# Kernel tuning notes

Hardware: AMD Instinct MI355X
Metric: run time of the kernel (lower is better)

The kernel has to match this reference:

```python
import jax, jax.numpy as jnp
import numpy as np

N_NODES = 100_000
N_EDGES = 1_600_000
N_GRAPHS = 512
D_NODE = 128
H = 128
L_EXTRA = 2  # model_layer - 1


def _bn(x, g, b, eps=1e-5):
    # BatchNorm1d, training-mode math (biased batch variance), eval dropout = identity
    mu = jnp.mean(x, axis=0)
    var = jnp.var(x, axis=0)
    return g * (x - mu) * jax.lax.rsqrt(var + eps) + b


def _gin_conv(x, src, dst, W1, b1, bng, bnb, W2, b2):
    # GINConv (eps=0): mlp(x + sum_{j->i} x_j); mlp = Lin -> BN -> ReLU -> Lin
    agg = jax.ops.segment_sum(x[src], dst, num_segments=x.shape[0])
    h = x + agg
    h = jax.nn.relu(_bn(h @ W1 + b1, bng, bnb))
    return h @ W2 + b2


def setup_inputs():
    key = jax.random.key(0)
    ks = jax.random.split(key, 24)
    s = 0.05
    d = {}
    d["x"] = jax.random.normal(ks[0], (N_NODES, D_NODE), dtype=jnp.float32)
    d["edge_index"] = jax.random.randint(ks[1], (2, N_EDGES), 0, N_NODES, dtype=jnp.int32)
    d["batch"] = jnp.sort(jax.random.randint(ks[2], (N_NODES,), 0, N_GRAPHS, dtype=jnp.int32))
    d["vn_emb"] = jax.random.normal(ks[3], (1, H)) * s
    # conv1 MLP: Linear(D_NODE, 2H) -> BN -> ReLU -> Linear(2H, H)
    d["c1_W1"] = jax.random.normal(ks[4], (D_NODE, 2 * H)) * s
    d["c1_b1"] = jnp.zeros((2 * H,))
    d["c1_bng"] = jnp.ones((2 * H,))
    d["c1_bnb"] = jnp.zeros((2 * H,))
    d["c1_W2"] = jax.random.normal(ks[5], (2 * H, H)) * s
    d["c1_b2"] = jnp.zeros((H,))
    d["bn1_g"] = jnp.ones((H,))
    d["bn1_b"] = jnp.zeros((H,))
    # stacked extra GIN layers (model_layer - 1)
    d["cW1"] = jax.random.normal(ks[6], (L_EXTRA, H, 2 * H)) * s
    d["cb1"] = jnp.zeros((L_EXTRA, 2 * H))
    d["cbng"] = jnp.ones((L_EXTRA, 2 * H))
    d["cbnb"] = jnp.zeros((L_EXTRA, 2 * H))
    d["cW2"] = jax.random.normal(ks[7], (L_EXTRA, 2 * H, H)) * s
    d["cb2"] = jnp.zeros((L_EXTRA, H))
    d["bns_g"] = jnp.ones((L_EXTRA, H))
    d["bns_b"] = jnp.zeros((L_EXTRA, H))
    # virtual node MLP: Lin(H,2H)->BN->ReLU->Lin(2H,H)->BN->ReLU->Dropout
    d["vW1"] = jax.random.normal(ks[8], (H, 2 * H)) * s
    d["vb1"] = jnp.zeros((2 * H,))
    d["vbn1_g"] = jnp.ones((2 * H,))
    d["vbn1_b"] = jnp.zeros((2 * H,))
    d["vW2"] = jax.random.normal(ks[9], (2 * H, H)) * s
    d["vb2"] = jnp.zeros((H,))
    d["vbn2_g"] = jnp.ones((H,))
    d["vbn2_b"] = jnp.zeros((H,))
    return d


def reference(x, edge_index, batch, vn_emb, c1_W1, c1_b1, c1_bng, c1_bnb, c1_W2, c1_b2,
              bn1_g, bn1_b, cW1, cb1, cbng, cbnb, cW2, cb2, bns_g, bns_b,
              vW1, vb1, vbn1_g, vbn1_b, vW2, vb2, vbn2_g, vbn2_b):
    src, dst = edge_index[0], edge_index[1]
    # virtual node feature per graph: Embedding(1, H) indexed with zeros
    vfeat = jnp.broadcast_to(vn_emb[0], (N_GRAPHS, H))
    # layer 1: dropout is identity in eval mode
    post = jax.nn.relu(_bn(_gin_conv(x, src, dst, c1_W1, c1_b1, c1_bng, c1_bnb, c1_W2, c1_b2), bn1_g, bn1_b))
    for i in range(L_EXTRA):
        post = post + vfeat[batch]                       # virtual-node broadcast
        post = _bn(_gin_conv(post, src, dst, cW1[i], cb1[i], cbng[i], cbnb[i], cW2[i], cb2[i]), bns_g[i], bns_b[i])
        if i < L_EXTRA - 1:
            post = jax.nn.relu(post)
            pooled = jax.ops.segment_sum(post, batch, num_segments=N_GRAPHS)  # GlobalAddPool
            z = pooled + vfeat
            z = jax.nn.relu(_bn(z @ vW1 + vb1, vbn1_g, vbn1_b))
            vfeat = jax.nn.relu(_bn(z @ vW2 + vb2, vbn2_g, vbn2_b))
    # readout: global mean pool over nodes per graph
    counts = jax.ops.segment_sum(jnp.ones((x.shape[0],), post.dtype), batch, num_segments=N_GRAPHS)
    out = jax.ops.segment_sum(post, batch, num_segments=N_GRAPHS) / jnp.maximum(counts, 1.0)[:, None]
    return out
```

## Files before the change

### kernel.cpp

```cpp
#include <hip/hip_runtime.h>

#define NN 100000
#define NE 1600000
#define NG 512
#define DH 128
#define DH2 256
#define SCB 98
#define NSTRIPE 32

typedef __attribute__((ext_vector_type(8))) _Float16 h8;
typedef __attribute__((ext_vector_type(2))) _Float16 h2;
typedef __attribute__((ext_vector_type(4))) float f4;

static inline size_t align256(size_t x) { return (x + 255) & ~size_t(255); }

__global__ __launch_bounds__(256) void countslot_k(const int* __restrict__ ei,
                                                   int* __restrict__ cursor,
                                                   int* __restrict__ slot) {
    int i = blockIdx.x * blockDim.x + threadIdx.x;
    int stride = gridDim.x * blockDim.x;
    for (int e = i; e < NE; e += stride)
        slot[e] = atomicAdd(&cursor[ei[NE + e]], 1);
}

__global__ __launch_bounds__(256) void place_k(const int* __restrict__ ei,
                                               const int* __restrict__ rowptr,
                                               const int* __restrict__ slot,
                                               int* __restrict__ esrc) {
    int i = blockIdx.x * blockDim.x + threadIdx.x;
    int stride = gridDim.x * blockDim.x;
    for (int e = i; e < NE; e += stride)
        esrc[rowptr[ei[NE + e]] + slot[e]] = ei[e];
}

__global__ void gbound_k(const int* __restrict__ batch, int* __restrict__ gcnt) {
    int g = blockIdx.x * blockDim.x + threadIdx.x;
    if (g >= NG) return;
    int lo = 0, hi = NN;
    while (lo < hi) { int m = (lo + hi) >> 1; if (batch[m] < g) lo = m + 1; else hi = m; }
    int b0 = lo;
    lo = 0; hi = NN;
    int g1 = g + 1;
    while (lo < hi) { int m = (lo + hi) >> 1; if (batch[m] < g1) lo = m + 1; else hi = m; }
    gcnt[g] = lo - b0;
}

__global__ __launch_bounds__(256) void scan1_k(const int* __restrict__ deg,
                                               int* __restrict__ part) {
    int i0 = blockIdx.x * 1024 + threadIdx.x * 4;
    int s = 0;
    if (i0 < NN) {
        int4 v = *(const int4*)(deg + i0);
        s = v.x + v.y + v.z + v.w;
    }
#pragma unroll
    for (int o = 1; o < 64; o <<= 1) s += __shfl_xor(s, o);
    __shared__ int ws[4];
    if ((threadIdx.x & 63) == 0) ws[threadIdx.x >> 6] = s;
    __syncthreads();
    if (threadIdx.x == 0) part[blockIdx.x] = ws[0] + ws[1] + ws[2] + ws[3];
}

__global__ void scan2_k(int* __restrict__ part, int* __restrict__ rowptr) {
    if (threadIdx.x == 0) {
        int run = 0;
        for (int i = 0; i < SCB; i++) { int v = part[i]; part[i] = run; run += v; }
        rowptr[NN] = run;
    }
}

__global__ __launch_bounds__(256) void scan3_k(const int* __restrict__ deg,
                                               const int* __restrict__ part,
                                               int* __restrict__ rowptr) {
    int t = threadIdx.x;
    int i0 = blockIdx.x * 1024 + t * 4;
    int4 v = {0, 0, 0, 0};
    if (i0 < NN) v = *(const int4*)(deg + i0);
    int s = v.x + v.y + v.z + v.w;
    __shared__ int sc[256];
    sc[t] = s;
    __syncthreads();
    for (int o = 1; o < 256; o <<= 1) {
        int add = (t >= o) ? sc[t - o] : 0;
        __syncthreads();
        sc[t] += add;
        __syncthreads();
    }
    int excl = (t ? sc[t - 1] : 0) + part[blockIdx.x];
    if (i0 < NN) {
        int4 r;
        r.x = excl;
        r.y = excl + v.x;
        r.z = excl + v.x + v.y;
        r.w = excl + v.x + v.y + v.z;
        *(int4*)(rowptr + i0) = r;
    }
}

__global__ void castx_k(const float* __restrict__ x, _Float16* __restrict__ xh) {
    int i = blockIdx.x * blockDim.x + threadIdx.x;
    if (i >= NN * 16) return;
    const float4* s = (const float4*)x + i * 2;
    float4 p = s[0], q = s[1];
    h8 h = {(_Float16)p.x, (_Float16)p.y, (_Float16)p.z, (_Float16)p.w,
            (_Float16)q.x, (_Float16)q.y, (_Float16)q.z, (_Float16)q.w};
    ((h8*)xh)[i] = h;
}

__global__ void vinit_k(const float* __restrict__ emb, _Float16* __restrict__ vfeat) {
    int i = blockIdx.x * blockDim.x + threadIdx.x;
    if (i < NG * DH) vfeat[i] = (_Float16)emb[i & (DH - 1)];
}

__global__ void zin_k(const float* __restrict__ pooled, const _Float16* __restrict__ vf,
                      _Float16* __restrict__ zb) {
    int i = blockIdx.x * blockDim.x + threadIdx.x;
    if (i < NG * DH) zb[i] = (_Float16)(pooled[i] + (float)vf[i]);
}

__global__ void addvn_k(_Float16* __restrict__ x, const _Float16* __restrict__ vfeat,
                        const int* __restrict__ batch) {
    int i = blockIdx.x * blockDim.x + threadIdx.x;
    if (i >= NN * 16) return;
    int row = i >> 4;
    int bg = batch[row];
    h8 u = ((h8*)x)[i];
    h8 v = ((const h8*)vfeat)[bg * 16 + (i & 15)];
    h8 o;
#pragma unroll
    for (int e = 0; e < 8; e++) o[e] = (_Float16)((float)u[e] + (float)v[e]);
    ((h8*)x)[i] = o;
}

__global__ void finalout_k(const float* __restrict__ pooled2, const int* __restrict__ gcnt,
                           float* __restrict__ outp) {
    int i = blockIdx.x * blockDim.x + threadIdx.x;
    if (i >= NG * DH) return;
    float cnt = (float)gcnt[i >> 7];
    outp[i] = pooled2[i] / fmaxf(cnt, 1.0f);
}

__global__ void bnfin_k(const float* __restrict__ csum, const float* __restrict__ csq,
                        const float* __restrict__ g, const float* __restrict__ b,
                        float* __restrict__ scale, float* __restrict__ shift,
                        int NC, int M) {
    int col = threadIdx.x;
    if (col >= NC) return;
    float s = 0.f, q = 0.f;
    for (int st = 0; st < NSTRIPE; st++) { s += csum[st * NC + col]; q += csq[st * NC + col]; }
    float invM = 1.0f / (float)M;
    float mean = s * invM;
    float var = q * invM - mean * mean;
    float sc = g[col] * rsqrtf(var + 1e-5f);
    scale[col] = sc;
    shift[col] = b[col] - mean * sc;
}

struct WPack {
    const float* w[8];
    _Float16* wt[8];
    int K[8];
    int N[8];
};
__global__ void wtrans_k(WPack p) {
    int id = blockIdx.z;
    const float* W = p.w[id];
    _Float16* Wt = p.wt[id];
    int K = p.K[id], N = p.N[id];
    int n0 = blockIdx.x * 32, k0 = blockIdx.y * 32;
    if (n0 >= N || k0 >= K) return;
    __shared__ float t[32][33];
    int tx = threadIdx.x & 31, ty = threadIdx.x >> 5;
    for (int i = 0; i < 32; i += 8)
        t[ty + i][tx] = W[(size_t)(k0 + ty + i) * N + n0 + tx];
    __syncthreads();
    for (int i = 0; i < 32; i += 8)
        Wt[(size_t)(n0 + ty + i) * K + k0 + tx] = (_Float16)t[tx][ty + i];
}

__global__ __launch_bounds__(256) void agg_k(const _Float16* __restrict__ xin,
                                             const int* __restrict__ rowptr,
                                             const int* __restrict__ esrc,
                                             _Float16* __restrict__ out) {
    int wave = threadIdx.x >> 6, lane = threadIdx.x & 63;
    int node = blockIdx.x * 4 + wave;
    if (node >= NN) return;
    const h2* xr = (const h2*)xin;
    h2 self = xr[(size_t)node * 64 + lane];
    float a0 = (float)self.x, a1 = (float)self.y;
    int beg = rowptr[node], end = rowptr[node + 1];
    int j = beg;
    for (; j + 3 < end; j += 4) {
        int s0 = esrc[j], s1 = esrc[j + 1], s2 = esrc[j + 2], s3 = esrc[j + 3];
        h2 u0 = xr[(size_t)s0 * 64 + lane];
        h2 u1 = xr[(size_t)s1 * 64 + lane];
        h2 u2 = xr[(size_t)s2 * 64 + lane];
        h2 u3 = xr[(size_t)s3 * 64 + lane];
        a0 += (float)u0.x + (float)u1.x + (float)u2.x + (float)u3.x;
        a1 += (float)u0.y + (float)u1.y + (float)u2.y + (float)u3.y;
    }
    for (; j < end; j++) {
        h2 u = xr[(size_t)esrc[j] * 64 + lane];
        a0 += (float)u.x; a1 += (float)u.y;
    }
    h2 o; o.x = (_Float16)a0; o.y = (_Float16)a1;
    ((h2*)out)[(size_t)node * 64 + lane] = o;
}

template <int K, int NCF>
__global__ __launch_bounds__(256, 2) void mgemm_k(
        const _Float16* __restrict__ A, const _Float16* __restrict__ Wt,
        const float* __restrict__ bias, _Float16* __restrict__ C,
        float* __restrict__ csum, float* __restrict__ csq, int M,
        const float* __restrict__ bnsc, const float* __restrict__ bnsh) {
    constexpr int BK = 128;
    constexpr int LDA = BK + 8;
    __shared__ __align__(16) _Float16 As[128 * LDA];
    const int tid = threadIdx.x;
    const int lane = tid & 63;
    const int wave = tid >> 6;
    const int wr = wave & 1, wc = wave >> 1;
    const int lm = lane & 15, lq = lane >> 4;
    const int mB = blockIdx.x * 128;
    const int n0 = blockIdx.y * 128 + wc * 64;

    f4 acc[4][4];
#pragma unroll
    for (int i = 0; i < 4; i++)
#pragma unroll
        for (int j = 0; j < 4; j++) acc[i][j] = (f4){0.f, 0.f, 0.f, 0.f};

    const int sr = tid >> 4;
    const int sc = (tid & 15) * 8;

    for (int kc = 0; kc < K; kc += BK) {
        if (kc) __syncthreads();
        float bscv[8], bshv[8];
        if (bnsc) {
            float4 s0 = *(const float4*)&bnsc[kc + sc];
            float4 s1 = *(const float4*)&bnsc[kc + sc + 4];
            float4 t0 = *(const float4*)&bnsh[kc + sc];
            float4 t1 = *(const float4*)&bnsh[kc + sc + 4];
            bscv[0] = s0.x; bscv[1] = s0.y; bscv[2] = s0.z; bscv[3] = s0.w;
            bscv[4] = s1.x; bscv[5] = s1.y; bscv[6] = s1.z; bscv[7] = s1.w;
            bshv[0] = t0.x; bshv[1] = t0.y; bshv[2] = t0.z; bshv[3] = t0.w;
            bshv[4] = t1.x; bshv[5] = t1.y; bshv[6] = t1.z; bshv[7] = t1.w;
        }
#pragma unroll
        for (int rr = 0; rr < 128; rr += 16) {
            int gr = mB + rr + sr; if (gr >= M) gr = M - 1;
            h8 h = *(const h8*)&A[(size_t)gr * K + kc + sc];
            if (bnsc) {
#pragma unroll
                for (int e = 0; e < 8; e++)
                    h[e] = (_Float16)fmaxf((float)h[e] * bscv[e] + bshv[e], 0.f);
            }
            *(h8*)&As[(rr + sr) * LDA + sc] = h;
        }
        __syncthreads();
#pragma unroll
        for (int ks = 0; ks < BK / 32; ks++) {
            h8 af[4], bf[4];
#pragma unroll
            for (int t = 0; t < 4; t++) {
                af[t] = *(const h8*)&As[(wr * 64 + t * 16 + lm) * LDA + ks * 32 + lq * 8];
                bf[t] = *(const h8*)&Wt[(size_t)(n0 + t * 16 + lm) * K + kc + ks * 32 + lq * 8];
            }
#pragma unroll
            for (int i = 0; i < 4; i++)
#pragma unroll
                for (int j = 0; j < 4; j++)
                    acc[i][j] = __builtin_amdgcn_mfma_f32_16x16x32_f16(af[i], bf[j], acc[i][j], 0, 0, 0);
        }
    }

    float bv[4];
#pragma unroll
    for (int j = 0; j < 4; j++) bv[j] = bias[n0 + j * 16 + lm];
    float ls[4] = {0, 0, 0, 0}, lsq[4] = {0, 0, 0, 0};
    __syncthreads();
    _Float16* Cs = As;
#pragma unroll
    for (int i = 0; i < 4; i++) {
        int row = wr * 64 + i * 16 + lq * 4;
        bool rv[4];
#pragma unroll
        for (int r = 0; r < 4; r++) rv[r] = (mB + row + r) < M;
#pragma unroll
        for (int j = 0; j < 4; j++) {
#pragma unroll
            for (int r = 0; r < 4; r++) {
                float v = acc[i][j][r] + bv[j];
                Cs[(row + r) * LDA + wc * 64 + j * 16 + lm] = (_Float16)v;
                if (rv[r]) { ls[j] += v; lsq[j] += v * v; }
            }
        }
    }
    const int stripe = blockIdx.x & (NSTRIPE - 1);
#pragma unroll
    for (int j = 0; j < 4; j++) {
        float s = ls[j], q = lsq[j];
        s += __shfl_xor(s, 16); s += __shfl_xor(s, 32);
        q += __shfl_xor(q, 16); q += __shfl_xor(q, 32);
        if (lq == 0) {
            atomicAdd(&csum[stripe * NCF + n0 + j * 16 + lm], s);
            atomicAdd(&csq[stripe * NCF + n0 + j * 16 + lm], q);
        }
    }
    __syncthreads();
    const int trow = tid >> 4;
    const int tcol = (tid & 15) * 8;
    const int cb = blockIdx.y * 128;
#pragma unroll
    for (int p = 0; p < 8; p++) {
        int row = p * 16 + trow;
        int grow = mB + row;
        if (grow < M) {
            h8 v = *(const h8*)&Cs[row * LDA + tcol];
            *(h8*)&C[(size_t)grow * NCF + cb + tcol] = v;
        }
    }
}

__global__ void bnrelu_k(const _Float16* __restrict__ in, _Float16* __restrict__ out,
                         const float* __restrict__ scale, const float* __restrict__ shift,
                         const _Float16* __restrict__ vfeat, const int* __restrict__ batch,
                         int M) {
    constexpr int PER = 16;
    int tid = blockIdx.x * blockDim.x + threadIdx.x;
    int c8 = tid % PER;
    int c0 = c8 * 8;
    float sc[8], sh[8];
    float4 s0 = *(const float4*)&scale[c0];
    float4 s1 = *(const float4*)&scale[c0 + 4];
    float4 t0 = *(const float4*)&shift[c0];
    float4 t1 = *(const float4*)&shift[c0 + 4];
    sc[0] = s0.x; sc[1] = s0.y; sc[2] = s0.z; sc[3] = s0.w;
    sc[4] = s1.x; sc[5] = s1.y; sc[6] = s1.z; sc[7] = s1.w;
    sh[0] = t0.x; sh[1] = t0.y; sh[2] = t0.z; sh[3] = t0.w;
    sh[4] = t1.x; sh[5] = t1.y; sh[6] = t1.z; sh[7] = t1.w;
    int total = M * PER;
    int stride = gridDim.x * blockDim.x;
    for (int i = tid; i < total; i += stride) {
        int row = i / PER;
        h8 u = ((const h8*)in)[i];
        h8 w;
        bool vn = (vfeat != nullptr);
        if (vn) w = ((const h8*)vfeat)[batch[row] * PER + c8];
        h8 o;
#pragma unroll
        for (int e = 0; e < 8; e++) {
            float vv = fmaxf((float)u[e] * sc[e] + sh[e], 0.f);
            if (vn) vv += (float)w[e];
            o[e] = (_Float16)vv;
        }
        ((h8*)out)[i] = o;
    }
}

__global__ __launch_bounds__(256) void bnpool_k(
        const _Float16* __restrict__ in, _Float16* __restrict__ out,
        const float* __restrict__ scale, const float* __restrict__ shift,
        const int* __restrict__ batch, float* __restrict__ pooled,
        int M, int relu) {
    int t = threadIdx.x;
    int c0 = (t & 63) * 2;
    int r0 = blockIdx.x * 128 + (t >> 6) * 32;
    float sc0 = scale[c0], h0 = shift[c0];
    float sc1 = scale[c0 + 1], h1 = shift[c0 + 1];
    int rend = r0 + 32; if (rend > M) rend = M;
    float a0 = 0.f, a1 = 0.f; int cur = -1;
    for (int r = r0; r < rend; r++) {
        h2 u = ((const h2*)in)[(size_t)r * 64 + (c0 >> 1)];
        float v0 = (float)u.x * sc0 + h0;
        float v1 = (float)u.y * sc1 + h1;
        if (relu) { v0 = fmaxf(v0, 0.f); v1 = fmaxf(v1, 0.f); }
        if (out) { h2 o; o.x = (_Float16)v0; o.y = (_Float16)v1; ((h2*)out)[(size_t)r * 64 + (c0 >> 1)] = o; }
        int bg = batch[r];
        if (bg != cur) {
            if (cur >= 0) {
                atomicAdd(&pooled[(size_t)cur * DH + c0], a0);
                atomicAdd(&pooled[(size_t)cur * DH + c0 + 1], a1);
            }
            cur = bg; a0 = 0.f; a1 = 0.f;
        }
        a0 += v0; a1 += v1;
    }
    if (cur >= 0) {
        atomicAdd(&pooled[(size_t)cur * DH + c0], a0);
        atomicAdd(&pooled[(size_t)cur * DH + c0 + 1], a1);
    }
}

extern "C" void kernel_launch(void* const* d_in, const int* in_sizes, int n_in,
                              void* d_out, int out_size, void* d_ws, size_t ws_size,
                              hipStream_t stream) {
    const float* x      = (const float*)d_in[0];
    const int*   ei     = (const int*)d_in[1];
    const int*   batch  = (const int*)d_in[2];
    const float* vn_emb = (const float*)d_in[3];
    const float* c1_W1  = (const float*)d_in[4];
    const float* c1_b1  = (const float*)d_in[5];
    const float* c1_bng = (const float*)d_in[6];
    const float* c1_bnb = (const float*)d_in[7];
    const float* c1_W2  = (const float*)d_in[8];
    const float* c1_b2  = (const float*)d_in[9];
    const float* bn1_g  = (const float*)d_in[10];
    const float* bn1_b  = (const float*)d_in[11];
    const float* cW1    = (const float*)d_in[12];
    const float* cb1    = (const float*)d_in[13];
    const float* cbng   = (const float*)d_in[14];
    const float* cbnb   = (const float*)d_in[15];
    const float* cW2    = (const float*)d_in[16];
    const float* cb2    = (const float*)d_in[17];
    const float* bns_g  = (const float*)d_in[18];
    const float* bns_b  = (const float*)d_in[19];
    const float* vW1    = (const float*)d_in[20];
    const float* vb1    = (const float*)d_in[21];
    const float* vbn1_g = (const float*)d_in[22];
    const float* vbn1_b = (const float*)d_in[23];
    const float* vW2    = (const float*)d_in[24];
    const float* vb2    = (const float*)d_in[25];
    const float* vbn2_g = (const float*)d_in[26];
    const float* vbn2_b = (const float*)d_in[27];
    float* outp = (float*)d_out;
    (void)in_sizes; (void)n_in; (void)out_size; (void)ws_size;

    char* w = (char*)d_ws;
    size_t off = 0;
    auto carve = [&](size_t bytes) -> void* {
        void* p = w + off; off = align256(off + bytes); return p;
    };
    int*   cursor  = (int*)carve((size_t)NN * 4);
    float* pooled  = (float*)carve((size_t)NG * DH * 4);
    float* pooled2 = (float*)carve((size_t)NG * DH * 4);
    float *sA[3], *qA[3], *sB[3], *qB[3], *sV1, *qV1, *sV2, *qV2;
    for (int i = 0; i < 3; i++) {
        sA[i] = (float*)carve((size_t)NSTRIPE * 256 * 4);
        qA[i] = (float*)carve((size_t)NSTRIPE * 256 * 4);
    }
    for (int i = 0; i < 3; i++) {
        sB[i] = (float*)carve((size_t)NSTRIPE * 128 * 4);
        qB[i] = (float*)carve((size_t)NSTRIPE * 128 * 4);
    }
    sV1 = (float*)carve((size_t)NSTRIPE * 256 * 4);
    qV1 = (float*)carve((size_t)NSTRIPE * 256 * 4);
    sV2 = (float*)carve((size_t)NSTRIPE * 128 * 4);
    qV2 = (float*)carve((size_t)NSTRIPE * 128 * 4);
    size_t zbytes = off;
    float *scA[3], *shA[3], *scB[3], *shB[3];
    for (int i = 0; i < 3; i++) { scA[i] = (float*)carve(256 * 4); shA[i] = (float*)carve(256 * 4); }
    for (int i = 0; i < 3; i++) { scB[i] = (float*)carve(128 * 4); shB[i] = (float*)carve(128 * 4); }
    float* scV1 = (float*)carve(256 * 4); float* shV1 = (float*)carve(256 * 4);
    float* scV2 = (float*)carve(128 * 4); float* shV2 = (float*)carve(128 * 4);
    int*   gcnt    = (int*)carve((size_t)NG * 4);
    int*   rowptr  = (int*)carve((size_t)(NN + 1) * 4);
    int*   slot    = (int*)carve((size_t)NE * 4);
    int*   esrc    = (int*)carve((size_t)NE * 4);
    int*   part    = (int*)carve((size_t)SCB * 4);
    _Float16* vfeat = (_Float16*)carve((size_t)NG * DH * 2);
    _Float16* zin   = (_Float16*)carve((size_t)NG * DH * 2);
    _Float16* zb    = (_Float16*)carve((size_t)NG * DH2 * 2);
    _Float16* vraw  = (_Float16*)carve((size_t)NG * DH * 2);
    _Float16* xh    = (_Float16*)carve((size_t)NN * DH * 2);
    _Float16* hb    = (_Float16*)carve((size_t)NN * DH * 2);
    _Float16* b1    = (_Float16*)carve((size_t)NN * DH2 * 2);
    _Float16* abuf  = (_Float16*)carve((size_t)NN * DH * 2);
    _Float16* Wt[8];
    for (int i = 0; i < 8; i++) Wt[i] = (_Float16*)carve((size_t)DH * DH2 * 2);

    WPack wp;
    wp.w[0] = c1_W1;            wp.K[0] = 128; wp.N[0] = 256;
    wp.w[1] = c1_W2;            wp.K[1] = 256; wp.N[1] = 128;
    wp.w[2] = cW1;              wp.K[2] = 128; wp.N[2] = 256;
    wp.w[3] = cW2;              wp.K[3] = 256; wp.N[3] = 128;
    wp.w[4] = cW1 + 128 * 256;  wp.K[4] = 128; wp.N[4] = 256;
    wp.w[5] = cW2 + 256 * 128;  wp.K[5] = 256; wp.N[5] = 128;
    wp.w[6] = vW1;              wp.K[6] = 128; wp.N[6] = 256;
    wp.w[7] = vW2;              wp.K[7] = 256; wp.N[7] = 128;
    for (int i = 0; i < 8; i++) wp.wt[i] = Wt[i];

    const int GB = (NN + 127) / 128;
    dim3 gemmA(GB, 2), gemmB(GB, 1);
    const float* NUL = nullptr;

    hipMemsetAsync(d_ws, 0, zbytes, stream);
    countslot_k<<<782, 256, 0, stream>>>(ei, cursor, slot);
    scan1_k<<<SCB, 256, 0, stream>>>(cursor, part);
    scan2_k<<<1, 64, 0, stream>>>(part, rowptr);
    scan3_k<<<SCB, 256, 0, stream>>>(cursor, part, rowptr);
    place_k<<<782, 256, 0, stream>>>(ei, rowptr, slot, esrc);
    gbound_k<<<2, 256, 0, stream>>>(batch, gcnt);
    wtrans_k<<<dim3(8, 8, 8), 256, 0, stream>>>(wp);
    vinit_k<<<(NG * DH + 255) / 256, 256, 0, stream>>>(vn_emb, vfeat);
    castx_k<<<(NN * 16 + 255) / 256, 256, 0, stream>>>(x, xh);

    agg_k<<<NN / 4, 256, 0, stream>>>(xh, rowptr, esrc, hb);
    mgemm_k<128, 256><<<gemmA, 256, 0, stream>>>(hb, Wt[0], c1_b1, b1, sA[0], qA[0], NN, NUL, NUL);
    bnfin_k<<<1, 256, 0, stream>>>(sA[0], qA[0], c1_bng, c1_bnb, scA[0], shA[0], 256, NN);
    mgemm_k<256, 128><<<gemmB, 256, 0, stream>>>(b1, Wt[1], c1_b2, abuf, sB[0], qB[0], NN,
                                                 scA[0], shA[0]);
    bnfin_k<<<1, 256, 0, stream>>>(sB[0], qB[0], bn1_g, bn1_b, scB[0], shB[0], 128, NN);
    bnrelu_k<<<2048, 256, 0, stream>>>(abuf, abuf, scB[0], shB[0], vfeat, batch, NN);

    agg_k<<<NN / 4, 256, 0, stream>>>(abuf, rowptr, esrc, hb);
    mgemm_k<128, 256><<<gemmA, 256, 0, stream>>>(hb, Wt[2], cb1, b1, sA[1], qA[1], NN, NUL, NUL);
    bnfin_k<<<1, 256, 0, stream>>>(sA[1], qA[1], cbng, cbnb, scA[1], shA[1], 256, NN);
    mgemm_k<256, 128><<<gemmB, 256, 0, stream>>>(b1, Wt[3], cb2, abuf, sB[1], qB[1], NN,
                                                 scA[1], shA[1]);
    bnfin_k<<<1, 256, 0, stream>>>(sB[1], qB[1], bns_g, bns_b, scB[1], shB[1], 128, NN);
    bnpool_k<<<GB, 256, 0, stream>>>(abuf, abuf, scB[1], shB[1], batch, pooled, NN, 1);

    zin_k<<<(NG * DH + 255) / 256, 256, 0, stream>>>(pooled, vfeat, zin);
    mgemm_k<128, 256><<<dim3(4, 2), 256, 0, stream>>>(zin, Wt[6], vb1, zb, sV1, qV1, NG, NUL, NUL);
    bnfin_k<<<1, 256, 0, stream>>>(sV1, qV1, vbn1_g, vbn1_b, scV1, shV1, 256, NG);
    mgemm_k<256, 128><<<dim3(4, 1), 256, 0, stream>>>(zb, Wt[7], vb2, vraw, sV2, qV2, NG,
                                                      scV1, shV1);
    bnfin_k<<<1, 256, 0, stream>>>(sV2, qV2, vbn2_g, vbn2_b, scV2, shV2, 128, NG);
    bnrelu_k<<<32, 256, 0, stream>>>(vraw, vfeat, scV2, shV2, nullptr, nullptr, NG);

    addvn_k<<<(NN * 16 + 255) / 256, 256, 0, stream>>>(abuf, vfeat, batch);
    agg_k<<<NN / 4, 256, 0, stream>>>(abuf, rowptr, esrc, hb);
    mgemm_k<128, 256><<<gemmA, 256, 0, stream>>>(hb, Wt[4], cb1 + 256, b1, sA[2], qA[2], NN, NUL, NUL);
    bnfin_k<<<1, 256, 0, stream>>>(sA[2], qA[2], cbng + 256, cbnb + 256, scA[2], shA[2], 256, NN);
    mgemm_k<256, 128><<<gemmB, 256, 0, stream>>>(b1, Wt[5], cb2 + 128, abuf, sB[2], qB[2], NN,
                                                 scA[2], shA[2]);
    bnfin_k<<<1, 256, 0, stream>>>(sB[2], qB[2], bns_g + 128, bns_b + 128, scB[2], shB[2], 128, NN);
    bnpool_k<<<GB, 256, 0, stream>>>(abuf, nullptr, scB[2], shB[2], batch, pooled2, NN, 0);

    finalout_k<<<(NG * DH + 255) / 256, 256, 0, stream>>>(pooled2, gcnt, outp);
}
```

Measured before the change: 818.3 us.

## Fuse neighbor aggregation into first GIN linear layer GEMM

Replaces the separate wave-per-node aggregation kernel and the first MLP GEMM with one kernel. Each block gathers and sums neighbor rows for its 128 nodes directly into shared memory, then runs MFMA against both 128-column halves of W1, writing the output and the BN statistics. This removes the write and re-read of the aggregated buffer and one launch per layer. In exchange the gather phase runs with fewer parallel nodes per CU (16 threads per row, 8 rows per pass), so latency hiding for the random gathers may suffer.

```diff
diff --git a/kernel.cpp b/kernel.cpp
--- a/kernel.cpp
+++ b/kernel.cpp
@@ -178,33 +178,124 @@
         Wt[(size_t)(n0 + ty + i) * K + k0 + tx] = (_Float16)t[tx][ty + i];
 }
 
-__global__ __launch_bounds__(256) void agg_k(const _Float16* __restrict__ xin,
-                                             const int* __restrict__ rowptr,
-                                             const int* __restrict__ esrc,
-                                             _Float16* __restrict__ out) {
-    int wave = threadIdx.x >> 6, lane = threadIdx.x & 63;
-    int node = blockIdx.x * 4 + wave;
-    if (node >= NN) return;
-    const h2* xr = (const h2*)xin;
-    h2 self = xr[(size_t)node * 64 + lane];
-    float a0 = (float)self.x, a1 = (float)self.y;
-    int beg = rowptr[node], end = rowptr[node + 1];
-    int j = beg;
-    for (; j + 3 < end; j += 4) {
-        int s0 = esrc[j], s1 = esrc[j + 1], s2 = esrc[j + 2], s3 = esrc[j + 3];
-        h2 u0 = xr[(size_t)s0 * 64 + lane];
-        h2 u1 = xr[(size_t)s1 * 64 + lane];
-        h2 u2 = xr[(size_t)s2 * 64 + lane];
-        h2 u3 = xr[(size_t)s3 * 64 + lane];
-        a0 += (float)u0.x + (float)u1.x + (float)u2.x + (float)u3.x;
-        a1 += (float)u0.y + (float)u1.y + (float)u2.y + (float)u3.y;
-    }
-    for (; j < end; j++) {
-        h2 u = xr[(size_t)esrc[j] * 64 + lane];
-        a0 += (float)u.x; a1 += (float)u.y;
-    }
-    h2 o; o.x = (_Float16)a0; o.y = (_Float16)a1;
-    ((h2*)out)[(size_t)node * 64 + lane] = o;
+__global__ __launch_bounds__(256, 2) void aggemm_k(
+        const _Float16* __restrict__ X, const int* __restrict__ rowptr,
+        const int* __restrict__ esrc, const _Float16* __restrict__ Wt,
+        const float* __restrict__ bias, _Float16* __restrict__ C,
+        float* __restrict__ csum, float* __restrict__ csq, int M) {
+    constexpr int K = 128, NCF = 256;
+    constexpr int LDA = K + 8;
+    __shared__ __align__(16) _Float16 As[128 * LDA];
+    const int tid = threadIdx.x;
+    const int lane = tid & 63;
+    const int wave = tid >> 6;
+    const int wr = wave & 1, wc = wave >> 1;
+    const int lm = lane & 15, lq = lane >> 4;
+    const int mB = blockIdx.x * 128;
+
+    const int sr = tid >> 4;
+    const int sc = (tid & 15) * 8;
+
+#pragma unroll
+    for (int rr = 0; rr < 128; rr += 16) {
+        int gr = mB + rr + sr; if (gr >= M) gr = M - 1;
+        h8 u = *(const h8*)&X[(size_t)gr * K + sc];
+        float a[8];
+#pragma unroll
+        for (int e = 0; e < 8; e++) a[e] = (float)u[e];
+        int beg = rowptr[gr], end = rowptr[gr + 1];
+        int j = beg;
+        for (; j + 1 < end; j += 2) {
+            int s0 = esrc[j], s1 = esrc[j + 1];
+            h8 u0 = *(const h8*)&X[(size_t)s0 * K + sc];
+            h8 u1 = *(const h8*)&X[(size_t)s1 * K + sc];
+#pragma unroll
+            for (int e = 0; e < 8; e++) a[e] += (float)u0[e] + (float)u1[e];
+        }
+        if (j < end) {
+            h8 u0 = *(const h8*)&X[(size_t)esrc[j] * K + sc];
+#pragma unroll
+            for (int e = 0; e < 8; e++) a[e] += (float)u0[e];
+        }
+        h8 h;
+#pragma unroll
+        for (int e = 0; e < 8; e++) h[e] = (_Float16)a[e];
+        *(h8*)&As[(rr + sr) * LDA + sc] = h;
+    }
+    __syncthreads();
+
+    f4 acc[4][8];
+#pragma unroll
+    for (int i = 0; i < 4; i++)
+#pragma unroll
+        for (int jj = 0; jj < 8; jj++) acc[i][jj] = (f4){0.f, 0.f, 0.f, 0.f};
+#pragma unroll
+    for (int ct = 0; ct < 2; ct++) {
+        const int n0 = ct * 128 + wc * 64;
+#pragma unroll
+        for (int ks = 0; ks < 4; ks++) {
+            h8 af[4], bf[4];
+#pragma unroll
+            for (int t = 0; t < 4; t++) {
+                af[t] = *(const h8*)&As[(wr * 64 + t * 16 + lm) * LDA + ks * 32 + lq * 8];
+                bf[t] = *(const h8*)&Wt[(size_t)(n0 + t * 16 + lm) * K + ks * 32 + lq * 8];
+            }
+#pragma unroll
+            for (int i = 0; i < 4; i++)
+#pragma unroll
+                for (int j = 0; j < 4; j++)
+                    acc[i][ct * 4 + j] =
+                        __builtin_amdgcn_mfma_f32_16x16x32_f16(af[i], bf[j], acc[i][ct * 4 + j], 0, 0, 0);
+        }
+    }
+
+    float bv[8];
+#pragma unroll
+    for (int jj = 0; jj < 8; jj++) bv[jj] = bias[(jj >> 2) * 128 + wc * 64 + (jj & 3) * 16 + lm];
+    float ls[8] = {0, 0, 0, 0, 0, 0, 0, 0}, lsq[8] = {0, 0, 0, 0, 0, 0, 0, 0};
+    _Float16* Cs = As;
+    const int trow = tid >> 4;
+    const int tcol = (tid & 15) * 8;
+#pragma unroll
+    for (int half = 0; half < 2; half++) {
+        __syncthreads();
+#pragma unroll
+        for (int i = 0; i < 4; i++) {
+            int row = wr * 64 + i * 16 + lq * 4;
+#pragma unroll
+            for (int j = 0; j < 4; j++) {
+                int jj = half * 4 + j;
+#pragma unroll
+                for (int r = 0; r < 4; r++) {
+                    float v = acc[i][jj][r] + bv[jj];
+                    Cs[(row + r) * LDA + wc * 64 + j * 16 + lm] = (_Float16)v;
+                    if (mB + row + r < M) { ls[jj] += v; lsq[jj] += v * v; }
+                }
+            }
+        }
+        __syncthreads();
+#pragma unroll
+        for (int p = 0; p < 8; p++) {
+            int row = p * 16 + trow;
+            int grow = mB + row;
+            if (grow < M) {
+                h8 v = *(const h8*)&Cs[row * LDA + tcol];
+                *(h8*)&C[(size_t)grow * NCF + half * 128 + tcol] = v;
+            }
+        }
+    }
+    const int stripe = blockIdx.x & (NSTRIPE - 1);
+#pragma unroll
+    for (int jj = 0; jj < 8; jj++) {
+        float s = ls[jj], q = lsq[jj];
+        s += __shfl_xor(s, 16); s += __shfl_xor(s, 32);
+        q += __shfl_xor(q, 16); q += __shfl_xor(q, 32);
+        if (lq == 0) {
+            int col = (jj >> 2) * 128 + wc * 64 + (jj & 3) * 16 + lm;
+            atomicAdd(&csum[stripe * NCF + col], s);
+            atomicAdd(&csq[stripe * NCF + col], q);
+        }
+    }
 }
 
 template <int K, int NCF>
@@ -463,7 +554,6 @@
     _Float16* zb    = (_Float16*)carve((size_t)NG * DH2 * 2);
     _Float16* vraw  = (_Float16*)carve((size_t)NG * DH * 2);
     _Float16* xh    = (_Float16*)carve((size_t)NN * DH * 2);
-    _Float16* hb    = (_Float16*)carve((size_t)NN * DH * 2);
     _Float16* b1    = (_Float16*)carve((size_t)NN * DH2 * 2);
     _Float16* abuf  = (_Float16*)carve((size_t)NN * DH * 2);
     _Float16* Wt[8];
@@ -481,7 +571,7 @@
     for (int i = 0; i < 8; i++) wp.wt[i] = Wt[i];
 
     const int GB = (NN + 127) / 128;
-    dim3 gemmA(GB, 2), gemmB(GB, 1);
+    dim3 gemmB(GB, 1);
     const float* NUL = nullptr;
 
     hipMemsetAsync(d_ws, 0, zbytes, stream);
@@ -495,16 +585,14 @@
     vinit_k<<<(NG * DH + 255) / 256, 256, 0, stream>>>(vn_emb, vfeat);
     castx_k<<<(NN * 16 + 255) / 256, 256, 0, stream>>>(x, xh);
 
-    agg_k<<<NN / 4, 256, 0, stream>>>(xh, rowptr, esrc, hb);
-    mgemm_k<128, 256><<<gemmA, 256, 0, stream>>>(hb, Wt[0], c1_b1, b1, sA[0], qA[0], NN, NUL, NUL);
+    aggemm_k<<<GB, 256, 0, stream>>>(xh, rowptr, esrc, Wt[0], c1_b1, b1, sA[0], qA[0], NN);
     bnfin_k<<<1, 256, 0, stream>>>(sA[0], qA[0], c1_bng, c1_bnb, scA[0], shA[0], 256, NN);
     mgemm_k<256, 128><<<gemmB, 256, 0, stream>>>(b1, Wt[1], c1_b2, abuf, sB[0], qB[0], NN,
                                                  scA[0], shA[0]);
     bnfin_k<<<1, 256, 0, stream>>>(sB[0], qB[0], bn1_g, bn1_b, scB[0], shB[0], 128, NN);
     bnrelu_k<<<2048, 256, 0, stream>>>(abuf, abuf, scB[0], shB[0], vfeat, batch, NN);
 
-    agg_k<<<NN / 4, 256, 0, stream>>>(abuf, rowptr, esrc, hb);
-    mgemm_k<128, 256><<<gemmA, 256, 0, stream>>>(hb, Wt[2], cb1, b1, sA[1], qA[1], NN, NUL, NUL);
+    aggemm_k<<<GB, 256, 0, stream>>>(abuf, rowptr, esrc, Wt[2], cb1, b1, sA[1], qA[1], NN);
     bnfin_k<<<1, 256, 0, stream>>>(sA[1], qA[1], cbng, cbnb, scA[1], shA[1], 256, NN);
     mgemm_k<256, 128><<<gemmB, 256, 0, stream>>>(b1, Wt[3], cb2, abuf, sB[1], qB[1], NN,
                                                  scA[1], shA[1]);
@@ -520,8 +608,7 @@
     bnrelu_k<<<32, 256, 0, stream>>>(vraw, vfeat, scV2, shV2, nullptr, nullptr, NG);
 
     addvn_k<<<(NN * 16 + 255) / 256, 256, 0, stream>>>(abuf, vfeat, batch);
-    agg_k<<<NN / 4, 256, 0, stream>>>(abuf, rowptr, esrc, hb);
-    mgemm_k<128, 256><<<gemmA, 256, 0, stream>>>(hb, Wt[4], cb1 + 256, b1, sA[2], qA[2], NN, NUL, NUL);
+    aggemm_k<<<GB, 256, 0, stream>>>(abuf, rowptr, esrc, Wt[4], cb1 + 256, b1, sA[2], qA[2], NN);
     bnfin_k<<<1, 256, 0, stream>>>(sA[2], qA[2], cbng + 256, cbnb + 256, scA[2], shA[2], 256, NN);
     mgemm_k<256, 128><<<gemmB, 256, 0, stream>>>(b1, Wt[5], cb2 + 128, abuf, sB[2], qB[2], NN,
                                                  scA[2], shA[2]);
```

After: 984.1 us. 20.3% more time.
